# Optimization experiments

Measured on AMD Instinct MI355X. Metric: run time of the kernel, lower is better.

## Reference

```python
import jax, jax.numpy as jnp
import numpy as np

BATCH, SEQ, IN, HID, OUT = 128, 1024, 256, 1024, 256

def setup_inputs() -> dict:
    key = jax.random.key(0)
    ks = jax.random.split(key, 6)
    s_in = 1.0 / np.sqrt(IN)
    s_h = 1.0 / np.sqrt(HID)
    return {
        "x": jax.random.normal(ks[0], (BATCH, SEQ, IN), jnp.float32),
        "Wx": jax.random.normal(ks[1], (IN, 4 * HID), jnp.float32) * s_in,
        "Wh": jax.random.normal(ks[2], (HID, 4 * HID), jnp.float32) * s_h,
        "b": jax.random.normal(ks[3], (4 * HID,), jnp.float32) * 0.01,
        "Wfc": jax.random.normal(ks[4], (HID, OUT), jnp.float32) * s_h,
        "bfc": jax.random.normal(ks[5], (OUT,), jnp.float32) * 0.01,
    }

def reference(x, Wx, Wh, b, Wfc, bfc):
    # Precompute input projections for all timesteps in one big GEMM: [B,S,4H]
    xg = jnp.einsum('bsi,ig->bsg', x, Wx) + b
    H = Wh.shape[0]
    B = x.shape[0]

    def step(carry, xg_t):
        h, c = carry
        gates = xg_t + h @ Wh  # [B, 4H]
        f = jax.nn.sigmoid(gates[:, 0*H:1*H])
        i = jax.nn.sigmoid(gates[:, 1*H:2*H])
        g = jnp.tanh(gates[:, 2*H:3*H])
        o = jax.nn.sigmoid(gates[:, 3*H:4*H])
        c_new = f * c + i * g
        h_new = o * jnp.tanh(c_new)
        return (h_new, c_new), None

    h0 = jnp.zeros((B, H), x.dtype)
    c0 = jnp.zeros((B, H), x.dtype)
    (h_T, _), _ = jax.lax.scan(step, (h0, c0), jnp.swapaxes(xg, 0, 1))
    return h_T @ Wfc + bfc
```

## Files before the change

kernel.cpp:

```cpp
#include <hip/hip_runtime.h>
#include <hip/hip_bf16.h>

#define BATCH 128
#define SEQ   1024
#define INDIM 256
#define HID   1024
#define NGATE 4096
#define KTOT  1280
#define OUTD  256
#define NKK   40
#define XKK   8
#define HKK   32
#define NBG   8
#define ROWS  16
#define NSL   32
#define JCOLS 32

typedef __attribute__((ext_vector_type(8))) short s16x8;
typedef __attribute__((ext_vector_type(4))) float f32x4;

__device__ __forceinline__ unsigned short f2bf(float f) {
    unsigned int u = __float_as_uint(f);
    u += 0x7FFFu + ((u >> 16) & 1u);
    return (unsigned short)(u >> 16);
}
__device__ __forceinline__ float sigmoidf_(float x) {
    return 1.0f / (1.0f + __expf(-x));
}
__device__ __forceinline__ float tanhf_(float x) {
    return 1.0f - 2.0f / (1.0f + __expf(2.0f * x));
}


__global__ __launch_bounds__(256) void prep_wt(const float* __restrict__ Wx,
                                               const float* __restrict__ Wh,
                                               unsigned short* __restrict__ WT) {
    __shared__ float tile[64][65];
    int k0 = blockIdx.x * 64;
    int n0 = blockIdx.y * 64;
    for (int idx = threadIdx.x; idx < 64 * 64; idx += 256) {
        int kk = idx >> 6, nn = idx & 63;
        int k = k0 + kk;
        float v = (k < INDIM) ? Wx[(size_t)k * NGATE + (n0 + nn)]
                              : Wh[(size_t)(k - INDIM) * NGATE + (n0 + nn)];
        tile[kk][nn] = v;
    }
    __syncthreads();
    for (int idx = threadIdx.x; idx < 64 * 64; idx += 256) {
        int nn = idx >> 6, kk = idx & 63;
        WT[(size_t)(n0 + nn) * KTOT + (k0 + kk)] = f2bf(tile[kk][nn]);
    }
}

__global__ __launch_bounds__(256) void prep_x(const float* __restrict__ x,
                                              unsigned short* __restrict__ xb,
                                              unsigned short* __restrict__ h0,
                                              unsigned int* __restrict__ flags) {
    int gid = blockIdx.x * blockDim.x + threadIdx.x;
    int stride = gridDim.x * blockDim.x;
    const int N4 = BATCH * SEQ * INDIM / 4;
    const float4* xv = reinterpret_cast<const float4*>(x);
    uint2* xo = reinterpret_cast<uint2*>(xb);
    for (int i = gid; i < N4; i += stride) {
        float4 v = xv[i];
        uint2 o;
        o.x = (unsigned)f2bf(v.x) | ((unsigned)f2bf(v.y) << 16);
        o.y = (unsigned)f2bf(v.z) | ((unsigned)f2bf(v.w) << 16);
        xo[i] = o;
    }
    const int NH = BATCH * HID;
    for (int i = gid; i < NH; i += stride) h0[i] = 0;
    for (int i = gid; i < 256 * 64; i += stride) flags[i] = 0;
}

__global__ __launch_bounds__(256, 1) void lstm_persist(
    const unsigned short* __restrict__ xb,
    const unsigned short* __restrict__ WT,
    unsigned short* __restrict__ h0,
    unsigned short* __restrict__ h1,
    unsigned int* __restrict__ flags,
    const float* __restrict__ bias) {

    __shared__ unsigned short xbuf[2][XKK * 512];
    __shared__ unsigned short hbuf[HKK * 512];
    __shared__ float gex[4 * ROWS * JCOLS];

    const int tid  = threadIdx.x;
    const int wave = tid >> 6, lane = tid & 63;
    const int lr = lane & 15, kq = lane >> 4;
    const int bg = blockIdx.x & 7;
    const int ns = blockIdx.x >> 3;
    const int b0 = bg * ROWS;
    const int j0 = ns * JCOLS;

    s16x8 b0r[NKK], b1r[NKK];
    {
        const unsigned short* base0 =
            WT + ((size_t)(wave * HID + j0 + lr)) * KTOT + kq * 8;
        const unsigned short* base1 = base0 + (size_t)16 * KTOT;
#pragma unroll
        for (int kk = 0; kk < NKK; kk++) {
            b0r[kk] = *reinterpret_cast<const s16x8*>(base0 + kk * 32);
            b1r[kk] = *reinterpret_cast<const s16x8*>(base1 + kk * 32);
        }
    }

    const int ecol = tid & 31, erow0 = tid >> 5, erow1 = erow0 + 8;
    const int j = j0 + ecol;
    const float bf = bias[0 * HID + j], bi = bias[1 * HID + j],
                bgg = bias[2 * HID + j], bo = bias[3 * HID + j];
    float c0 = 0.f, c1 = 0.f;

    const int srow = lane >> 2;
    const int skq = ((lane & 3) - ((lane >> 3) & 3)) & 3;
    const unsigned short* xsrc =
        xb + (size_t)(b0 + srow) * SEQ * INDIM + skq * 8;
    const int p_l = lr * 4 + ((kq + (lr >> 1)) & 3);

    unsigned int* myflag = flags + (size_t)(bg * NSL + ns) * 64;

#pragma unroll
    for (int q = 0; q < 2; q++) {
        int kk = 2 * wave + q;
        __builtin_amdgcn_global_load_lds(
            (const __attribute__((address_space(1))) void*)(xsrc + (size_t)0 * INDIM + kk * 32),
            (__attribute__((address_space(3))) void*)(&xbuf[0][kk * 512]),
            16, 0, 0);
    }
    __syncthreads();

    for (int t = 0; t < SEQ; t++) {
        const unsigned short* hin = (t & 1) ? h1 : h0;
        unsigned short* hout      = (t & 1) ? h0 : h1;
        const int par = t & 1;

        f32x4 acc0 = {0.f, 0.f, 0.f, 0.f};
        f32x4 acc1 = {0.f, 0.f, 0.f, 0.f};
        {
            const unsigned short* ax = &xbuf[par][p_l * 8];
#pragma unroll
            for (int kk = 0; kk < XKK; kk++) {
                s16x8 a = *reinterpret_cast<const s16x8*>(ax + kk * 512);
                acc0 = __builtin_amdgcn_mfma_f32_16x16x32_bf16(a, b0r[kk], acc0, 0, 0, 0);
                acc1 = __builtin_amdgcn_mfma_f32_16x16x32_bf16(a, b1r[kk], acc1, 0, 0, 0);
            }
        }

        if (t + 1 < SEQ) {
#pragma unroll
            for (int q = 0; q < 2; q++) {
                int kk = 2 * wave + q;
                __builtin_amdgcn_global_load_lds(
                    (const __attribute__((address_space(1))) void*)(xsrc + (size_t)(t + 1) * INDIM + kk * 32),
                    (__attribute__((address_space(3))) void*)(&xbuf[par ^ 1][kk * 512]),
                    16, 0, 0);
            }
        }

        if (tid < NSL) {
            const unsigned int* fp = flags + (size_t)(bg * NSL + tid) * 64;
            while (__hip_atomic_load(fp, __ATOMIC_RELAXED,
                                     __HIP_MEMORY_SCOPE_AGENT) < (unsigned)t) {
                __builtin_amdgcn_s_sleep(1);
            }
        }
        asm volatile("" ::: "memory");
        __syncthreads();

        {
            unsigned long long hv[16];
#pragma unroll
            for (int i = 0; i < 16; i++) {
                int u = tid + 256 * i;
                int kkh = u >> 7, v = u & 127, row = v >> 3, k8 = v & 7;
                const unsigned long long* gp = (const unsigned long long*)
                    (hin + (size_t)(b0 + row) * HID + kkh * 32 + k8 * 4);
                hv[i] = __hip_atomic_load(gp, __ATOMIC_RELAXED,
                                          __HIP_MEMORY_SCOPE_AGENT);
            }
#pragma unroll
            for (int i = 0; i < 16; i++) {
                int u = tid + 256 * i;
                int kkh = u >> 7, v = u & 127, row = v >> 3, k8 = v & 7;
                int kqh = k8 >> 1;
                int p = row * 4 + ((kqh + (row >> 1)) & 3);
                *(unsigned long long*)((char*)hbuf + kkh * 1024 + p * 16 + (k8 & 1) * 8) = hv[i];
            }
        }
        __syncthreads();

        {
            const unsigned short* ah = &hbuf[p_l * 8];
#pragma unroll
            for (int kk = 0; kk < HKK; kk++) {
                s16x8 a = *reinterpret_cast<const s16x8*>(ah + kk * 512);
                acc0 = __builtin_amdgcn_mfma_f32_16x16x32_bf16(a, b0r[XKK + kk], acc0, 0, 0, 0);
                acc1 = __builtin_amdgcn_mfma_f32_16x16x32_bf16(a, b1r[XKK + kk], acc1, 0, 0, 0);
            }
        }

#pragma unroll
        for (int r = 0; r < 4; r++) {
            int row = kq * 4 + r;
            gex[wave * 512 + row * 32 + lr]      = acc0[r];
            gex[wave * 512 + row * 32 + 16 + lr] = acc1[r];
        }
        __syncthreads();

        {
            float ff = sigmoidf_(gex[0 * 512 + erow0 * 32 + ecol] + bf);
            float ii = sigmoidf_(gex[1 * 512 + erow0 * 32 + ecol] + bi);
            float gg = tanhf_(gex[2 * 512 + erow0 * 32 + ecol] + bgg);
            float oo = sigmoidf_(gex[3 * 512 + erow0 * 32 + ecol] + bo);
            c0 = ff * c0 + ii * gg;
            __hip_atomic_store(hout + (size_t)(b0 + erow0) * HID + j,
                               f2bf(oo * tanhf_(c0)),
                               __ATOMIC_RELAXED, __HIP_MEMORY_SCOPE_AGENT);
        }
        {
            float ff = sigmoidf_(gex[0 * 512 + erow1 * 32 + ecol] + bf);
            float ii = sigmoidf_(gex[1 * 512 + erow1 * 32 + ecol] + bi);
            float gg = tanhf_(gex[2 * 512 + erow1 * 32 + ecol] + bgg);
            float oo = sigmoidf_(gex[3 * 512 + erow1 * 32 + ecol] + bo);
            c1 = ff * c1 + ii * gg;
            __hip_atomic_store(hout + (size_t)(b0 + erow1) * HID + j,
                               f2bf(oo * tanhf_(c1)),
                               __ATOMIC_RELAXED, __HIP_MEMORY_SCOPE_AGENT);
        }

        __syncthreads();
        asm volatile("" ::: "memory");
        if (tid == 0) {
            __hip_atomic_store(myflag, (unsigned)(t + 1),
                               __ATOMIC_RELAXED, __HIP_MEMORY_SCOPE_AGENT);
        }
    }
}

__global__ __launch_bounds__(256) void final_fc(const unsigned short* __restrict__ h,
                                                const float* __restrict__ Wfc,
                                                const float* __restrict__ bfc,
                                                float* __restrict__ out) {
    int b = blockIdx.x;
    int o = threadIdx.x;
    const unsigned short* hr = h + (size_t)b * HID;
    float acc = bfc[o];
#pragma unroll 8
    for (int k = 0; k < HID; k++) {
        acc += __uint_as_float(((unsigned)hr[k]) << 16) * Wfc[(size_t)k * OUTD + o];
    }
    out[(size_t)b * OUTD + o] = acc;
}

extern "C" void kernel_launch(void* const* d_in, const int* in_sizes, int n_in,
                              void* d_out, int out_size, void* d_ws, size_t ws_size,
                              hipStream_t stream) {
    const float* x    = (const float*)d_in[0];
    const float* Wx   = (const float*)d_in[1];
    const float* Wh   = (const float*)d_in[2];
    const float* bias = (const float*)d_in[3];
    const float* Wfc  = (const float*)d_in[4];
    const float* bfc  = (const float*)d_in[5];
    float* out = (float*)d_out;

    char* ws = (char*)d_ws;
    unsigned short* WT  = (unsigned short*)(ws);
    unsigned short* xb  = (unsigned short*)(ws + 10485760);
    unsigned short* h0  = (unsigned short*)(ws + 77594624);
    unsigned short* h1  = (unsigned short*)(ws + 77856768);
    unsigned int* flags = (unsigned int*)(ws + 78118912);

    hipLaunchKernelGGL(prep_wt, dim3(KTOT / 64, NGATE / 64), dim3(256), 0, stream,
                       Wx, Wh, WT);
    hipLaunchKernelGGL(prep_x, dim3(1024), dim3(256), 0, stream, x, xb, h0, flags);

    hipLaunchKernelGGL(lstm_persist, dim3(256), dim3(256), 0, stream,
                       xb, WT, h0, h1, flags, bias);

    hipLaunchKernelGGL(final_fc, dim3(128), dim3(256), 0, stream, h0, Wfc, bfc, out);
}
```

Before: 3.563 ms.

## Replace per-block step flags with step tags packed into each h word

Each hidden-state value is now stored as a 32-bit word: the bf16 value in the low half and the step index in the high half. Consumers poll the h words directly until every tag matches the expected step. This removes the separate flag array, the trailing block barrier and the flag store/poll round trip from the recurrence's critical path. In exchange the h buffers double in size, so per-step global traffic for h grows, and the spin loop re-reads whole groups of words until they are current.

Result: slower. 4.305 ms (+20.8%).

```diff
diff --git a/kernel.cpp b/kernel.cpp
--- a/kernel.cpp
+++ b/kernel.cpp
@@ -31,7 +31,6 @@
     return 1.0f - 2.0f / (1.0f + __expf(2.0f * x));
 }
 
-
 __global__ __launch_bounds__(256) void prep_wt(const float* __restrict__ Wx,
                                                const float* __restrict__ Wh,
                                                unsigned short* __restrict__ WT) {
@@ -54,8 +53,8 @@
 
 __global__ __launch_bounds__(256) void prep_x(const float* __restrict__ x,
                                               unsigned short* __restrict__ xb,
-                                              unsigned short* __restrict__ h0,
-                                              unsigned int* __restrict__ flags) {
+                                              unsigned int* __restrict__ h0,
+                                              unsigned int* __restrict__ h1) {
     int gid = blockIdx.x * blockDim.x + threadIdx.x;
     int stride = gridDim.x * blockDim.x;
     const int N4 = BATCH * SEQ * INDIM / 4;
@@ -69,19 +68,21 @@
         xo[i] = o;
     }
     const int NH = BATCH * HID;
-    for (int i = gid; i < NH; i += stride) h0[i] = 0;
-    for (int i = gid; i < 256 * 64; i += stride) flags[i] = 0;
+    for (int i = gid; i < NH; i += stride) {
+        h0[i] = 0u;
+        h1[i] = 0xFFFF0000u;
+    }
 }
 
 __global__ __launch_bounds__(256, 1) void lstm_persist(
     const unsigned short* __restrict__ xb,
     const unsigned short* __restrict__ WT,
-    unsigned short* __restrict__ h0,
-    unsigned short* __restrict__ h1,
-    unsigned int* __restrict__ flags,
+    unsigned int* __restrict__ h0,
+    unsigned int* __restrict__ h1,
     const float* __restrict__ bias) {
 
-    __shared__ unsigned short xbuf[2][XKK * 512];
+    __shared__ unsigned short xbuf0[XKK * 512];
+    __shared__ unsigned short xbuf1[XKK * 512];
     __shared__ unsigned short hbuf[HKK * 512];
     __shared__ float gex[4 * ROWS * JCOLS];
 
@@ -117,27 +118,32 @@
         xb + (size_t)(b0 + srow) * SEQ * INDIM + skq * 8;
     const int p_l = lr * 4 + ((kq + (lr >> 1)) & 3);
 
-    unsigned int* myflag = flags + (size_t)(bg * NSL + ns) * 64;
+    const int hrow = tid >> 4, hk4 = tid & 15;
+    const int hkq = hk4 >> 2;
+    const int hp = hrow * 4 + ((hkq + (hrow >> 1)) & 3);
+    unsigned int* hb32 = (unsigned int*)hbuf;
+    const int hdst = hp * 4 + (hk4 & 3);
+    const size_t hsrc = (size_t)(b0 + hrow) * (HID / 2) + hk4;
 
 #pragma unroll
     for (int q = 0; q < 2; q++) {
         int kk = 2 * wave + q;
         __builtin_amdgcn_global_load_lds(
-            (const __attribute__((address_space(1))) void*)(xsrc + (size_t)0 * INDIM + kk * 32),
-            (__attribute__((address_space(3))) void*)(&xbuf[0][kk * 512]),
-            16, 0, 0);
+            (const __attribute__((address_space(1))) void*)(xsrc + (size_t)kk * 32),
+            (__attribute__((address_space(3))) void*)(xbuf0 + kk * 512), 16, 0, 0);
     }
     __syncthreads();
 
     for (int t = 0; t < SEQ; t++) {
-        const unsigned short* hin = (t & 1) ? h1 : h0;
-        unsigned short* hout      = (t & 1) ? h0 : h1;
-        const int par = t & 1;
+        const unsigned int* hin = (t & 1) ? h1 : h0;
+        unsigned int* hout      = (t & 1) ? h0 : h1;
+        unsigned short* xcur    = (t & 1) ? xbuf1 : xbuf0;
+        unsigned short* xnxt    = (t & 1) ? xbuf0 : xbuf1;
 
         f32x4 acc0 = {0.f, 0.f, 0.f, 0.f};
         f32x4 acc1 = {0.f, 0.f, 0.f, 0.f};
         {
-            const unsigned short* ax = &xbuf[par][p_l * 8];
+            const unsigned short* ax = xcur + p_l * 8;
 #pragma unroll
             for (int kk = 0; kk < XKK; kk++) {
                 s16x8 a = *reinterpret_cast<const s16x8*>(ax + kk * 512);
@@ -152,45 +158,52 @@
                 int kk = 2 * wave + q;
                 __builtin_amdgcn_global_load_lds(
                     (const __attribute__((address_space(1))) void*)(xsrc + (size_t)(t + 1) * INDIM + kk * 32),
-                    (__attribute__((address_space(3))) void*)(&xbuf[par ^ 1][kk * 512]),
-                    16, 0, 0);
-            }
-        }
-
-        if (tid < NSL) {
-            const unsigned int* fp = flags + (size_t)(bg * NSL + tid) * 64;
-            while (__hip_atomic_load(fp, __ATOMIC_RELAXED,
-                                     __HIP_MEMORY_SCOPE_AGENT) < (unsigned)t) {
-                __builtin_amdgcn_s_sleep(1);
-            }
-        }
-        asm volatile("" ::: "memory");
+                    (__attribute__((address_space(3))) void*)(xnxt + kk * 512), 16, 0, 0);
+            }
+        }
+
+        {
+            const unsigned long long* src =
+                (const unsigned long long*)hin + hsrc;
+            const unsigned exp = (unsigned)t;
+            unsigned long long w[4][8];
+#pragma unroll
+            for (int g = 0; g < 4; g++)
+#pragma unroll
+                for (int i = 0; i < 8; i++)
+                    w[g][i] = __hip_atomic_load(src + (size_t)(g * 8 + i) * 16,
+                                                __ATOMIC_RELAXED,
+                                                __HIP_MEMORY_SCOPE_AGENT);
+#pragma unroll
+            for (int g = 0; g < 4; g++) {
+                for (;;) {
+                    unsigned ok = 1u;
+#pragma unroll
+                    for (int i = 0; i < 8; i++) {
+                        unsigned hi = (unsigned)(w[g][i] >> 48);
+                        unsigned mid = (unsigned)(w[g][i] >> 16) & 0xFFFFu;
+                        ok &= (unsigned)(hi == exp) & (unsigned)(mid == exp);
+                    }
+                    if (ok) break;
+#pragma unroll
+                    for (int i = 0; i < 8; i++)
+                        w[g][i] = __hip_atomic_load(src + (size_t)(g * 8 + i) * 16,
+                                                    __ATOMIC_RELAXED,
+                                                    __HIP_MEMORY_SCOPE_AGENT);
+                }
+#pragma unroll
+                for (int i = 0; i < 8; i++) {
+                    int sl = g * 8 + i;
+                    unsigned lo = (unsigned)w[g][i];
+                    unsigned hi2 = (unsigned)(w[g][i] >> 32);
+                    hb32[sl * 256 + hdst] = (lo & 0xFFFFu) | (hi2 << 16);
+                }
+            }
+        }
         __syncthreads();
 
         {
-            unsigned long long hv[16];
-#pragma unroll
-            for (int i = 0; i < 16; i++) {
-                int u = tid + 256 * i;
-                int kkh = u >> 7, v = u & 127, row = v >> 3, k8 = v & 7;
-                const unsigned long long* gp = (const unsigned long long*)
-                    (hin + (size_t)(b0 + row) * HID + kkh * 32 + k8 * 4);
-                hv[i] = __hip_atomic_load(gp, __ATOMIC_RELAXED,
-                                          __HIP_MEMORY_SCOPE_AGENT);
-            }
-#pragma unroll
-            for (int i = 0; i < 16; i++) {
-                int u = tid + 256 * i;
-                int kkh = u >> 7, v = u & 127, row = v >> 3, k8 = v & 7;
-                int kqh = k8 >> 1;
-                int p = row * 4 + ((kqh + (row >> 1)) & 3);
-                *(unsigned long long*)((char*)hbuf + kkh * 1024 + p * 16 + (k8 & 1) * 8) = hv[i];
-            }
-        }
-        __syncthreads();
-
-        {
-            const unsigned short* ah = &hbuf[p_l * 8];
+            const unsigned short* ah = hbuf + p_l * 8;
 #pragma unroll
             for (int kk = 0; kk < HKK; kk++) {
                 s16x8 a = *reinterpret_cast<const s16x8*>(ah + kk * 512);
@@ -207,14 +220,15 @@
         }
         __syncthreads();
 
+        const unsigned otag = (unsigned)(t + 1) << 16;
         {
             float ff = sigmoidf_(gex[0 * 512 + erow0 * 32 + ecol] + bf);
             float ii = sigmoidf_(gex[1 * 512 + erow0 * 32 + ecol] + bi);
             float gg = tanhf_(gex[2 * 512 + erow0 * 32 + ecol] + bgg);
             float oo = sigmoidf_(gex[3 * 512 + erow0 * 32 + ecol] + bo);
             c0 = ff * c0 + ii * gg;
-            __hip_atomic_store(hout + (size_t)(b0 + erow0) * HID + j,
-                               f2bf(oo * tanhf_(c0)),
+            unsigned word = otag | (unsigned)f2bf(oo * tanhf_(c0));
+            __hip_atomic_store(hout + (size_t)(b0 + erow0) * HID + j, word,
                                __ATOMIC_RELAXED, __HIP_MEMORY_SCOPE_AGENT);
         }
         {
@@ -223,31 +237,24 @@
             float gg = tanhf_(gex[2 * 512 + erow1 * 32 + ecol] + bgg);
             float oo = sigmoidf_(gex[3 * 512 + erow1 * 32 + ecol] + bo);
             c1 = ff * c1 + ii * gg;
-            __hip_atomic_store(hout + (size_t)(b0 + erow1) * HID + j,
-                               f2bf(oo * tanhf_(c1)),
+            unsigned word = otag | (unsigned)f2bf(oo * tanhf_(c1));
+            __hip_atomic_store(hout + (size_t)(b0 + erow1) * HID + j, word,
                                __ATOMIC_RELAXED, __HIP_MEMORY_SCOPE_AGENT);
         }
-
-        __syncthreads();
-        asm volatile("" ::: "memory");
-        if (tid == 0) {
-            __hip_atomic_store(myflag, (unsigned)(t + 1),
-                               __ATOMIC_RELAXED, __HIP_MEMORY_SCOPE_AGENT);
-        }
-    }
-}
-
-__global__ __launch_bounds__(256) void final_fc(const unsigned short* __restrict__ h,
+    }
+}
+
+__global__ __launch_bounds__(256) void final_fc(const unsigned int* __restrict__ h,
                                                 const float* __restrict__ Wfc,
                                                 const float* __restrict__ bfc,
                                                 float* __restrict__ out) {
     int b = blockIdx.x;
     int o = threadIdx.x;
-    const unsigned short* hr = h + (size_t)b * HID;
+    const unsigned int* hr = h + (size_t)b * HID;
     float acc = bfc[o];
 #pragma unroll 8
     for (int k = 0; k < HID; k++) {
-        acc += __uint_as_float(((unsigned)hr[k]) << 16) * Wfc[(size_t)k * OUTD + o];
+        acc += __uint_as_float(hr[k] << 16) * Wfc[(size_t)k * OUTD + o];
     }
     out[(size_t)b * OUTD + o] = acc;
 }
@@ -264,18 +271,17 @@
     float* out = (float*)d_out;
 
     char* ws = (char*)d_ws;
-    unsigned short* WT  = (unsigned short*)(ws);
-    unsigned short* xb  = (unsigned short*)(ws + 10485760);
-    unsigned short* h0  = (unsigned short*)(ws + 77594624);
-    unsigned short* h1  = (unsigned short*)(ws + 77856768);
-    unsigned int* flags = (unsigned int*)(ws + 78118912);
+    unsigned short* WT = (unsigned short*)(ws);
+    unsigned short* xb = (unsigned short*)(ws + 10485760);
+    unsigned int* h0   = (unsigned int*)(ws + 77594624);
+    unsigned int* h1   = (unsigned int*)(ws + 78118912);
 
     hipLaunchKernelGGL(prep_wt, dim3(KTOT / 64, NGATE / 64), dim3(256), 0, stream,
                        Wx, Wh, WT);
-    hipLaunchKernelGGL(prep_x, dim3(1024), dim3(256), 0, stream, x, xb, h0, flags);
+    hipLaunchKernelGGL(prep_x, dim3(1024), dim3(256), 0, stream, x, xb, h0, h1);
 
     hipLaunchKernelGGL(lstm_persist, dim3(256), dim3(256), 0, stream,
-                       xb, WT, h0, h1, flags, bias);
+                       xb, WT, h0, h1, bias);
 
     hipLaunchKernelGGL(final_fc, dim3(128), dim3(256), 0, stream, h0, Wfc, bfc, out);
 }
```

## Retile persistent LSTM blocks to 32 rows by 16 columns with split-K waves

Applied to the files above, without the earlier changes.

Changes the per-block tile from 16 batch rows by 32 hidden columns to 32 rows by 16 columns. There are now 4 batch groups of 64 column slices instead of 8 groups of 32. Each wave handles two gate pairs over half of K and issues four MFMAs per loaded A fragment, so each A fragment is reused across both M tiles. Partial sums from the two K halves are reduced through padded shared memory, and the weight registers are pinned to AGPRs. Each block now waits on 64 peer flags instead of 32 and loads twice as much h per step. The goal is to cut per-block weight register pressure and LDS reads per MFMA.

Result: slower. 4.167 ms (+17.0%).

```diff
diff --git a/kernel.cpp b/kernel.cpp
--- a/kernel.cpp
+++ b/kernel.cpp
@@ -8,13 +8,12 @@
 #define NGATE 4096
 #define KTOT  1280
 #define OUTD  256
-#define NKK   40
+#define NBG   4
+#define ROWS  32
+#define NSL   64
+#define JCOLS 16
 #define XKK   8
 #define HKK   32
-#define NBG   8
-#define ROWS  16
-#define NSL   32
-#define JCOLS 32
 
 typedef __attribute__((ext_vector_type(8))) short s16x8;
 typedef __attribute__((ext_vector_type(4))) float f32x4;
@@ -30,7 +29,6 @@
 __device__ __forceinline__ float tanhf_(float x) {
     return 1.0f - 2.0f / (1.0f + __expf(2.0f * x));
 }
-
 
 __global__ __launch_bounds__(256) void prep_wt(const float* __restrict__ Wx,
                                                const float* __restrict__ Wh,
@@ -70,7 +68,7 @@
     }
     const int NH = BATCH * HID;
     for (int i = gid; i < NH; i += stride) h0[i] = 0;
-    for (int i = gid; i < 256 * 64; i += stride) flags[i] = 0;
+    for (int i = gid; i < 16384; i += stride) flags[i] = 0;
 }
 
 __global__ __launch_bounds__(256, 1) void lstm_persist(
@@ -81,50 +79,64 @@
     unsigned int* __restrict__ flags,
     const float* __restrict__ bias) {
 
-    __shared__ unsigned short xbuf[2][XKK * 512];
-    __shared__ unsigned short hbuf[HKK * 512];
-    __shared__ float gex[4 * ROWS * JCOLS];
+    __shared__ unsigned short xbuf[2][16 * 512];
+    __shared__ unsigned short hbuf[64 * 512];
+    __shared__ float gex2[2][32][68];
 
     const int tid  = threadIdx.x;
     const int wave = tid >> 6, lane = tid & 63;
     const int lr = lane & 15, kq = lane >> 4;
-    const int bg = blockIdx.x & 7;
-    const int ns = blockIdx.x >> 3;
-    const int b0 = bg * ROWS;
-    const int j0 = ns * JCOLS;
-
-    s16x8 b0r[NKK], b1r[NKK];
+    const int g  = blockIdx.x >> 6;
+    const int i  = blockIdx.x & 63;
+    const int b0 = g * ROWS;
+    const int j0 = i * JCOLS;
+    const int np = wave & 1;
+    const int kh = wave >> 1;
+
+    s16x8 bA[20], bB[20];
     {
-        const unsigned short* base0 =
-            WT + ((size_t)(wave * HID + j0 + lr)) * KTOT + kq * 8;
-        const unsigned short* base1 = base0 + (size_t)16 * KTOT;
-#pragma unroll
-        for (int kk = 0; kk < NKK; kk++) {
-            b0r[kk] = *reinterpret_cast<const s16x8*>(base0 + kk * 32);
-            b1r[kk] = *reinterpret_cast<const s16x8*>(base1 + kk * 32);
-        }
-    }
-
-    const int ecol = tid & 31, erow0 = tid >> 5, erow1 = erow0 + 8;
-    const int j = j0 + ecol;
-    const float bf = bias[0 * HID + j], bi = bias[1 * HID + j],
-                bgg = bias[2 * HID + j], bo = bias[3 * HID + j];
+        const unsigned short* baseA =
+            WT + ((size_t)((2 * np) * HID + j0 + lr)) * KTOT + kq * 8;
+        const unsigned short* baseB = baseA + (size_t)HID * KTOT;
+#pragma unroll
+        for (int idx = 0; idx < 4; idx++) {
+            int off = (kh * 4 + idx) * 32;
+            bA[idx] = *reinterpret_cast<const s16x8*>(baseA + off);
+            bB[idx] = *reinterpret_cast<const s16x8*>(baseB + off);
+        }
+#pragma unroll
+        for (int idx = 4; idx < 20; idx++) {
+            int off = INDIM + (kh * 16 + (idx - 4)) * 32;
+            bA[idx] = *reinterpret_cast<const s16x8*>(baseA + off);
+            bB[idx] = *reinterpret_cast<const s16x8*>(baseB + off);
+        }
+    }
+#pragma unroll
+    for (int q = 0; q < 20; q++) {
+        asm volatile("" : "+a"(bA[q]));
+        asm volatile("" : "+a"(bB[q]));
+    }
+
+    const int hcol = tid & 15, row0 = tid >> 4, row1 = row0 + 16;
+    const int j = j0 + hcol;
+    const float bf_ = bias[0 * HID + j], bi_ = bias[1 * HID + j],
+                bg_ = bias[2 * HID + j], bo_ = bias[3 * HID + j];
     float c0 = 0.f, c1 = 0.f;
 
-    const int srow = lane >> 2;
+    const int srow4 = lane >> 2;
     const int skq = ((lane & 3) - ((lane >> 3) & 3)) & 3;
     const unsigned short* xsrc =
-        xb + (size_t)(b0 + srow) * SEQ * INDIM + skq * 8;
+        xb + (size_t)(b0 + np * 16 + srow4) * SEQ * INDIM + skq * 8;
     const int p_l = lr * 4 + ((kq + (lr >> 1)) & 3);
 
-    unsigned int* myflag = flags + (size_t)(bg * NSL + ns) * 64;
-
-#pragma unroll
-    for (int q = 0; q < 2; q++) {
-        int kk = 2 * wave + q;
+    unsigned int* myflag = flags + (size_t)(g * NSL + i) * 64;
+
+#pragma unroll
+    for (int r = 0; r < 4; r++) {
+        int ks = 2 * r + kh;
         __builtin_amdgcn_global_load_lds(
-            (const __attribute__((address_space(1))) void*)(xsrc + (size_t)0 * INDIM + kk * 32),
-            (__attribute__((address_space(3))) void*)(&xbuf[0][kk * 512]),
+            (const __attribute__((address_space(1))) void*)(xsrc + (size_t)ks * 32),
+            (__attribute__((address_space(3))) void*)(&xbuf[0][(ks * 2 + np) * 512]),
             16, 0, 0);
     }
     __syncthreads();
@@ -134,31 +146,35 @@
         unsigned short* hout      = (t & 1) ? h0 : h1;
         const int par = t & 1;
 
-        f32x4 acc0 = {0.f, 0.f, 0.f, 0.f};
-        f32x4 acc1 = {0.f, 0.f, 0.f, 0.f};
-        {
-            const unsigned short* ax = &xbuf[par][p_l * 8];
-#pragma unroll
-            for (int kk = 0; kk < XKK; kk++) {
-                s16x8 a = *reinterpret_cast<const s16x8*>(ax + kk * 512);
-                acc0 = __builtin_amdgcn_mfma_f32_16x16x32_bf16(a, b0r[kk], acc0, 0, 0, 0);
-                acc1 = __builtin_amdgcn_mfma_f32_16x16x32_bf16(a, b1r[kk], acc1, 0, 0, 0);
+        f32x4 a00 = {0.f, 0.f, 0.f, 0.f}, a01 = {0.f, 0.f, 0.f, 0.f};
+        f32x4 a10 = {0.f, 0.f, 0.f, 0.f}, a11 = {0.f, 0.f, 0.f, 0.f};
+        {
+            const unsigned short* axb = &xbuf[par][p_l * 8];
+#pragma unroll
+            for (int idx = 0; idx < 4; idx++) {
+                int xks = kh * 4 + idx;
+                s16x8 am0 = *reinterpret_cast<const s16x8*>(axb + (xks * 2 + 0) * 512);
+                s16x8 am1 = *reinterpret_cast<const s16x8*>(axb + (xks * 2 + 1) * 512);
+                a00 = __builtin_amdgcn_mfma_f32_16x16x32_bf16(am0, bA[idx], a00, 0, 0, 0);
+                a01 = __builtin_amdgcn_mfma_f32_16x16x32_bf16(am0, bB[idx], a01, 0, 0, 0);
+                a10 = __builtin_amdgcn_mfma_f32_16x16x32_bf16(am1, bA[idx], a10, 0, 0, 0);
+                a11 = __builtin_amdgcn_mfma_f32_16x16x32_bf16(am1, bB[idx], a11, 0, 0, 0);
             }
         }
 
         if (t + 1 < SEQ) {
 #pragma unroll
-            for (int q = 0; q < 2; q++) {
-                int kk = 2 * wave + q;
+            for (int r = 0; r < 4; r++) {
+                int ks = 2 * r + kh;
                 __builtin_amdgcn_global_load_lds(
-                    (const __attribute__((address_space(1))) void*)(xsrc + (size_t)(t + 1) * INDIM + kk * 32),
-                    (__attribute__((address_space(3))) void*)(&xbuf[par ^ 1][kk * 512]),
+                    (const __attribute__((address_space(1))) void*)(xsrc + (size_t)(t + 1) * INDIM + ks * 32),
+                    (__attribute__((address_space(3))) void*)(&xbuf[par ^ 1][(ks * 2 + np) * 512]),
                     16, 0, 0);
             }
         }
 
-        if (tid < NSL) {
-            const unsigned int* fp = flags + (size_t)(bg * NSL + tid) * 64;
+        if (tid < 64) {
+            const unsigned int* fp = flags + (size_t)(g * NSL + tid) * 64;
             while (__hip_atomic_load(fp, __ATOMIC_RELAXED,
                                      __HIP_MEMORY_SCOPE_AGENT) < (unsigned)t) {
                 __builtin_amdgcn_s_sleep(1);
@@ -168,62 +184,81 @@
         __syncthreads();
 
         {
-            unsigned long long hv[16];
-#pragma unroll
-            for (int i = 0; i < 16; i++) {
-                int u = tid + 256 * i;
-                int kkh = u >> 7, v = u & 127, row = v >> 3, k8 = v & 7;
-                const unsigned long long* gp = (const unsigned long long*)
-                    (hin + (size_t)(b0 + row) * HID + kkh * 32 + k8 * 4);
-                hv[i] = __hip_atomic_load(gp, __ATOMIC_RELAXED,
-                                          __HIP_MEMORY_SCOPE_AGENT);
-            }
-#pragma unroll
-            for (int i = 0; i < 16; i++) {
-                int u = tid + 256 * i;
-                int kkh = u >> 7, v = u & 127, row = v >> 3, k8 = v & 7;
-                int kqh = k8 >> 1;
-                int p = row * 4 + ((kqh + (row >> 1)) & 3);
-                *(unsigned long long*)((char*)hbuf + kkh * 1024 + p * 16 + (k8 & 1) * 8) = hv[i];
+            const unsigned long long* hin_u = (const unsigned long long*)hin;
+#pragma unroll
+            for (int half = 0; half < 2; half++) {
+                unsigned long long hv[16];
+#pragma unroll
+                for (int q = 0; q < 16; q++) {
+                    int v = tid + 256 * (half * 16 + q);
+                    int hks = v >> 8, w8 = v & 255, row = w8 >> 3, k8 = w8 & 7;
+                    hv[q] = __hip_atomic_load(
+                        hin_u + (size_t)(b0 + row) * 256 + hks * 8 + k8,
+                        __ATOMIC_RELAXED, __HIP_MEMORY_SCOPE_AGENT);
+                }
+#pragma unroll
+                for (int q = 0; q < 16; q++) {
+                    int v = tid + 256 * (half * 16 + q);
+                    int hks = v >> 8, w8 = v & 255, row = w8 >> 3, k8 = w8 & 7;
+                    int r16 = row & 15, mt = row >> 4, kq2 = k8 >> 1;
+                    int p = r16 * 4 + ((kq2 + (r16 >> 1)) & 3);
+                    *(unsigned long long*)((char*)hbuf + (hks * 2 + mt) * 1024 +
+                                           p * 16 + (k8 & 1) * 8) = hv[q];
+                }
             }
         }
         __syncthreads();
 
         {
-            const unsigned short* ah = &hbuf[p_l * 8];
-#pragma unroll
-            for (int kk = 0; kk < HKK; kk++) {
-                s16x8 a = *reinterpret_cast<const s16x8*>(ah + kk * 512);
-                acc0 = __builtin_amdgcn_mfma_f32_16x16x32_bf16(a, b0r[XKK + kk], acc0, 0, 0, 0);
-                acc1 = __builtin_amdgcn_mfma_f32_16x16x32_bf16(a, b1r[XKK + kk], acc1, 0, 0, 0);
-            }
-        }
-
-#pragma unroll
-        for (int r = 0; r < 4; r++) {
-            int row = kq * 4 + r;
-            gex[wave * 512 + row * 32 + lr]      = acc0[r];
-            gex[wave * 512 + row * 32 + 16 + lr] = acc1[r];
+            const unsigned short* ahb = &hbuf[p_l * 8];
+#pragma unroll
+            for (int idx = 4; idx < 20; idx++) {
+                int hks = kh * 16 + (idx - 4);
+                s16x8 am0 = *reinterpret_cast<const s16x8*>(ahb + (hks * 2 + 0) * 512);
+                s16x8 am1 = *reinterpret_cast<const s16x8*>(ahb + (hks * 2 + 1) * 512);
+                a00 = __builtin_amdgcn_mfma_f32_16x16x32_bf16(am0, bA[idx], a00, 0, 0, 0);
+                a01 = __builtin_amdgcn_mfma_f32_16x16x32_bf16(am0, bB[idx], a01, 0, 0, 0);
+                a10 = __builtin_amdgcn_mfma_f32_16x16x32_bf16(am1, bA[idx], a10, 0, 0, 0);
+                a11 = __builtin_amdgcn_mfma_f32_16x16x32_bf16(am1, bB[idx], a11, 0, 0, 0);
+            }
+        }
+
+        {
+            float* gx = &gex2[kh][0][0];
+            const int ci0 = (np * 2 + 0) * 17 + lr;
+            const int ci1 = (np * 2 + 1) * 17 + lr;
+#pragma unroll
+            for (int r = 0; r < 4; r++) {
+                int row = kq * 4 + r;
+                gx[row * 68 + ci0]        = a00[r];
+                gx[row * 68 + ci1]        = a01[r];
+                gx[(row + 16) * 68 + ci0] = a10[r];
+                gx[(row + 16) * 68 + ci1] = a11[r];
+            }
         }
         __syncthreads();
 
         {
-            float ff = sigmoidf_(gex[0 * 512 + erow0 * 32 + ecol] + bf);
-            float ii = sigmoidf_(gex[1 * 512 + erow0 * 32 + ecol] + bi);
-            float gg = tanhf_(gex[2 * 512 + erow0 * 32 + ecol] + bgg);
-            float oo = sigmoidf_(gex[3 * 512 + erow0 * 32 + ecol] + bo);
-            c0 = ff * c0 + ii * gg;
-            __hip_atomic_store(hout + (size_t)(b0 + erow0) * HID + j,
+            float gf = gex2[0][row0][0 * 17 + hcol] + gex2[1][row0][0 * 17 + hcol] + bf_;
+            float gi = gex2[0][row0][1 * 17 + hcol] + gex2[1][row0][1 * 17 + hcol] + bi_;
+            float gg = gex2[0][row0][2 * 17 + hcol] + gex2[1][row0][2 * 17 + hcol] + bg_;
+            float go = gex2[0][row0][3 * 17 + hcol] + gex2[1][row0][3 * 17 + hcol] + bo_;
+            float ff = sigmoidf_(gf), ii = sigmoidf_(gi);
+            float g2 = tanhf_(gg), oo = sigmoidf_(go);
+            c0 = ff * c0 + ii * g2;
+            __hip_atomic_store(hout + (size_t)(b0 + row0) * HID + j,
                                f2bf(oo * tanhf_(c0)),
                                __ATOMIC_RELAXED, __HIP_MEMORY_SCOPE_AGENT);
         }
         {
-            float ff = sigmoidf_(gex[0 * 512 + erow1 * 32 + ecol] + bf);
-            float ii = sigmoidf_(gex[1 * 512 + erow1 * 32 + ecol] + bi);
-            float gg = tanhf_(gex[2 * 512 + erow1 * 32 + ecol] + bgg);
-            float oo = sigmoidf_(gex[3 * 512 + erow1 * 32 + ecol] + bo);
-            c1 = ff * c1 + ii * gg;
-            __hip_atomic_store(hout + (size_t)(b0 + erow1) * HID + j,
+            float gf = gex2[0][row1][0 * 17 + hcol] + gex2[1][row1][0 * 17 + hcol] + bf_;
+            float gi = gex2[0][row1][1 * 17 + hcol] + gex2[1][row1][1 * 17 + hcol] + bi_;
+            float gg = gex2[0][row1][2 * 17 + hcol] + gex2[1][row1][2 * 17 + hcol] + bg_;
+            float go = gex2[0][row1][3 * 17 + hcol] + gex2[1][row1][3 * 17 + hcol] + bo_;
+            float ff = sigmoidf_(gf), ii = sigmoidf_(gi);
+            float g2 = tanhf_(gg), oo = sigmoidf_(go);
+            c1 = ff * c1 + ii * g2;
+            __hip_atomic_store(hout + (size_t)(b0 + row1) * HID + j,
                                f2bf(oo * tanhf_(c1)),
                                __ATOMIC_RELAXED, __HIP_MEMORY_SCOPE_AGENT);
         }
```

## Use per-wave completion flags and hoist h loads ahead of x MFMAs

Applied to the files above, without the earlier changes.

Each wave now publishes its own completion flag after waiting for its own stores, which removes the block-wide barrier before signalling. Every wave polls all 128 producer flags directly instead of having 32 threads poll and then barrier. The global h loads are issued before the x-projection MFMAs so their latency overlaps that compute. This adds four times as many flag polls per consumer and relies on vmcnt(0) plus relaxed atomics for ordering, which carries some memory-ordering risk. A barrier still follows the LDS stores of h, and the gex buffer reuse across timesteps loses the trailing syncthreads, which is a possible race.

Measured after the change: 5.383 ms. 51.1% more time.

```diff
diff --git a/kernel.cpp b/kernel.cpp
--- a/kernel.cpp
+++ b/kernel.cpp
@@ -30,7 +30,6 @@
 __device__ __forceinline__ float tanhf_(float x) {
     return 1.0f - 2.0f / (1.0f + __expf(2.0f * x));
 }
-
 
 __global__ __launch_bounds__(256) void prep_wt(const float* __restrict__ Wx,
                                                const float* __restrict__ Wh,
@@ -70,7 +69,7 @@
     }
     const int NH = BATCH * HID;
     for (int i = gid; i < NH; i += stride) h0[i] = 0;
-    for (int i = gid; i < 256 * 64; i += stride) flags[i] = 0;
+    for (int i = gid; i < 32768; i += stride) flags[i] = 0;
 }
 
 __global__ __launch_bounds__(256, 1) void lstm_persist(
@@ -117,13 +116,17 @@
         xb + (size_t)(b0 + srow) * SEQ * INDIM + skq * 8;
     const int p_l = lr * 4 + ((kq + (lr >> 1)) & 3);
 
-    unsigned int* myflag = flags + (size_t)(bg * NSL + ns) * 64;
+    unsigned int* wflag =
+        flags + ((size_t)(bg * NSL + ns) * 4 + wave) * 16;
+    const unsigned int* fpA =
+        flags + ((size_t)(bg * NSL + (lane & 31)) * 4 + (lane >> 5)) * 16;
+    const unsigned int* fpB = fpA + 2 * 16;
 
 #pragma unroll
     for (int q = 0; q < 2; q++) {
         int kk = 2 * wave + q;
         __builtin_amdgcn_global_load_lds(
-            (const __attribute__((address_space(1))) void*)(xsrc + (size_t)0 * INDIM + kk * 32),
+            (const __attribute__((address_space(1))) void*)(xsrc + (size_t)kk * 32),
             (__attribute__((address_space(3))) void*)(&xbuf[0][kk * 512]),
             16, 0, 0);
     }
@@ -133,6 +136,29 @@
         const unsigned short* hin = (t & 1) ? h1 : h0;
         unsigned short* hout      = (t & 1) ? h0 : h1;
         const int par = t & 1;
+
+        if (t > 0) {
+            for (;;) {
+                unsigned a = __hip_atomic_load(fpA, __ATOMIC_RELAXED,
+                                               __HIP_MEMORY_SCOPE_AGENT);
+                unsigned b = __hip_atomic_load(fpB, __ATOMIC_RELAXED,
+                                               __HIP_MEMORY_SCOPE_AGENT);
+                if (__all((int)(a >= (unsigned)t) & (int)(b >= (unsigned)t)))
+                    break;
+                __builtin_amdgcn_s_sleep(1);
+            }
+        }
+
+        unsigned long long hv[16];
+#pragma unroll
+        for (int i = 0; i < 16; i++) {
+            int u = tid + 256 * i;
+            int kkh = u >> 7, v = u & 127, row = v >> 3, k8 = v & 7;
+            const unsigned long long* gp = (const unsigned long long*)
+                (hin + (size_t)(b0 + row) * HID + kkh * 32 + k8 * 4);
+            hv[i] = __hip_atomic_load(gp, __ATOMIC_RELAXED,
+                                      __HIP_MEMORY_SCOPE_AGENT);
+        }
 
         f32x4 acc0 = {0.f, 0.f, 0.f, 0.f};
         f32x4 acc1 = {0.f, 0.f, 0.f, 0.f};
@@ -157,35 +183,13 @@
             }
         }
 
-        if (tid < NSL) {
-            const unsigned int* fp = flags + (size_t)(bg * NSL + tid) * 64;
-            while (__hip_atomic_load(fp, __ATOMIC_RELAXED,
-                                     __HIP_MEMORY_SCOPE_AGENT) < (unsigned)t) {
-                __builtin_amdgcn_s_sleep(1);
-            }
-        }
-        asm volatile("" ::: "memory");
-        __syncthreads();
-
-        {
-            unsigned long long hv[16];
-#pragma unroll
-            for (int i = 0; i < 16; i++) {
-                int u = tid + 256 * i;
-                int kkh = u >> 7, v = u & 127, row = v >> 3, k8 = v & 7;
-                const unsigned long long* gp = (const unsigned long long*)
-                    (hin + (size_t)(b0 + row) * HID + kkh * 32 + k8 * 4);
-                hv[i] = __hip_atomic_load(gp, __ATOMIC_RELAXED,
-                                          __HIP_MEMORY_SCOPE_AGENT);
-            }
-#pragma unroll
-            for (int i = 0; i < 16; i++) {
-                int u = tid + 256 * i;
-                int kkh = u >> 7, v = u & 127, row = v >> 3, k8 = v & 7;
-                int kqh = k8 >> 1;
-                int p = row * 4 + ((kqh + (row >> 1)) & 3);
-                *(unsigned long long*)((char*)hbuf + kkh * 1024 + p * 16 + (k8 & 1) * 8) = hv[i];
-            }
+#pragma unroll
+        for (int i = 0; i < 16; i++) {
+            int u = tid + 256 * i;
+            int kkh = u >> 7, v = u & 127, row = v >> 3, k8 = v & 7;
+            int kqh = k8 >> 1;
+            int p = row * 4 + ((kqh + (row >> 1)) & 3);
+            *(unsigned long long*)((char*)hbuf + kkh * 1024 + p * 16 + (k8 & 1) * 8) = hv[i];
         }
         __syncthreads();
 
@@ -228,12 +232,10 @@
                                __ATOMIC_RELAXED, __HIP_MEMORY_SCOPE_AGENT);
         }
 
-        __syncthreads();
-        asm volatile("" ::: "memory");
-        if (tid == 0) {
-            __hip_atomic_store(myflag, (unsigned)(t + 1),
+        asm volatile("s_waitcnt vmcnt(0)" ::: "memory");
+        if (lane == 0)
+            __hip_atomic_store(wflag, (unsigned)(t + 1),
                                __ATOMIC_RELAXED, __HIP_MEMORY_SCOPE_AGENT);
-        }
     }
 }
 
```
